# Optimization experiments

Hardware: AMD Instinct MI355X
Metric: run time of the kernel (lower is better)

The kernel has to match this reference:

```python
import jax, jax.numpy as jnp
import numpy as np

D_MODEL = 1024
D_HIDDEN = 4096
D_VOCAB = 32000
N_CTX = 2048
N_LAYERS = 8


def setup_inputs() -> dict:
    key = jax.random.key(0)
    ks = jax.random.split(key, 10)
    # scale params by 1/sqrt(fan_in) so softmax/logits are numerically sane
    s = 1.0 / np.sqrt(D_MODEL)
    sh = 1.0 / np.sqrt(D_HIDDEN)
    return {
        "tokens": jax.random.randint(ks[0], (N_CTX,), 0, D_VOCAB),
        "tok_emb": jax.random.normal(ks[1], (D_VOCAB, D_MODEL), jnp.float32) * s,
        "pos_emb": jax.random.normal(ks[2], (N_CTX, D_MODEL), jnp.float32) * s,
        "wqk": jax.random.normal(ks[3], (N_LAYERS, D_MODEL, D_MODEL), jnp.float32) * s,
        "wov": jax.random.normal(ks[4], (N_LAYERS, D_MODEL, D_MODEL), jnp.float32) * s,
        "w_up": jax.random.normal(ks[5], (N_LAYERS, D_HIDDEN, D_MODEL), jnp.float32) * s,
        "b_up": jax.random.normal(ks[6], (N_LAYERS, D_HIDDEN), jnp.float32) * 0.01,
        "w_down": jax.random.normal(ks[7], (N_LAYERS, D_MODEL, D_HIDDEN), jnp.float32) * sh,
        "b_down": jax.random.normal(ks[8], (N_LAYERS, D_MODEL), jnp.float32) * 0.01,
    }


def reference(tokens, tok_emb, pos_emb, wqk, wov, w_up, b_up, w_down, b_down):
    n = tokens.shape[0]
    # token + positional embedding  -> [n, d_model]
    x = tok_emb[tokens] + pos_emb[:n]
    # causal additive mask: -inf strictly above the diagonal
    idx = jnp.arange(n)
    mask = jnp.where(idx[None, :] > idx[:, None], -jnp.inf, 0.0).astype(x.dtype)
    for l in range(wqk.shape[0]):
        # MLP branch: relu(x W_up^T + b_up) W_down^T + b_down
        h = jnp.maximum(x @ w_up[l].T + b_up[l], 0.0) @ w_down[l].T + b_down[l]
        # attention branch: softmax(x Wqk x^T + M) x Wov
        scores = (x @ wqk[l]) @ x.T + mask          # [n, n]
        attn = jax.nn.softmax(scores, axis=-1) @ x @ wov[l]
        x = x + h + attn                             # parallel residual
    # tied unembedding -> logits [n, d_vocab]
    return x @ tok_emb.T
```

## Files before the change

kernel.cpp:

```cpp
#include <hip/hip_runtime.h>
#include <hip/hip_bf16.h>
#include <stdint.h>

#define DM 1024
#define DH 4096
#define DV 32000
#define NC 2048
#define NL 8

typedef float f32x4_t __attribute__((ext_vector_type(4)));
typedef __bf16 bf16x8_t __attribute__((ext_vector_type(8)));
typedef unsigned short u16x4_t __attribute__((ext_vector_type(4)));
typedef unsigned short u16x8_t __attribute__((ext_vector_type(8)));

typedef __attribute__((address_space(1))) void as1_void;
typedef __attribute__((address_space(3))) void as3_void;

__device__ __forceinline__ unsigned short f2bf(float f) {
  unsigned int u = __builtin_bit_cast(unsigned int, f);
  u += 0x7fffu + ((u >> 16) & 1u);
  return (unsigned short)(u >> 16);
}

__device__ __forceinline__ void gload_lds16(const void* g, void* l) {
  __builtin_amdgcn_global_load_lds((as1_void*)(void*)g, (as3_void*)l, 16, 0, 0);
}

template <int BNT, bool B_FP32, bool SPLIT, bool CAUSAL, bool CAUSAL_K,
          bool HAS_BIAS, bool RELU, bool OUT_BF16>
__device__ __forceinline__ void gemm_body(
    unsigned short* As, unsigned short* Bs, const unsigned short* __restrict__ A,
    const void* __restrict__ Bt, const float* __restrict__ bias,
    void* __restrict__ Cout, int M, int N, int lda, int Ks, int bx, int by,
    int koff, int zslice) {
  constexpr int BK = 64;
  constexpr int BN = BNT;
  constexpr int CPTA = 4;
  constexpr int CPTB = (BN * BK) / 2048;
  constexpr int NF = BN / 32;
  const int t = threadIdx.x;
  const int lane = t & 63;
  const int wid = t >> 6;
  const int wr = wid >> 1, wc = wid & 1;
  const int row0 = by * 128;
  const int col0 = bx * BN;

  if constexpr (CAUSAL) {
    if (col0 > row0 + 127) return;
  }

  int Kend = Ks;
  if constexpr (CAUSAL_K) {
    const int need = row0 + 128 - koff;
    Kend = need <= 0 ? 0 : (need >= Ks ? Ks : ((need + BK - 1) & ~(BK - 1)));
    if constexpr (SPLIT) {
      if (Kend <= 0) return;
    }
  }

  f32x4_t acc[4][NF];
#pragma unroll
  for (int m = 0; m < 4; m++)
#pragma unroll
    for (int n = 0; n < NF; n++) acc[m][n] = (f32x4_t){0.f, 0.f, 0.f, 0.f};

  for (int kt = 0; kt < Kend; kt += BK) {
    __syncthreads();
#pragma unroll
    for (int i = 0; i < CPTA; i++) {
      const int c = i * 256 + t;
      const int r = c >> 3;
      const int ko = ((c & 7) ^ (r & 7)) * 8;
      const unsigned short* g = A + (size_t)(row0 + r) * lda + koff + kt + ko;
      unsigned short* l = &As[(size_t)(i * 256 + wid * 64) * 8];
      gload_lds16(g, l);
    }
    if constexpr (B_FP32) {
      const float* Bf = (const float*)Bt;
#pragma unroll
      for (int i = 0; i < CPTB; i++) {
        const int c = i * 256 + t;
        const int r = c >> 3;
        const int ko = ((c & 7) ^ (r & 7)) * 8;
        const float* g = Bf + (size_t)(col0 + r) * lda + koff + kt + ko;
        const float4 f0 = *reinterpret_cast<const float4*>(g);
        const float4 f1 = *reinterpret_cast<const float4*>(g + 4);
        u16x8_t v;
        v[0] = f2bf(f0.x); v[1] = f2bf(f0.y); v[2] = f2bf(f0.z); v[3] = f2bf(f0.w);
        v[4] = f2bf(f1.x); v[5] = f2bf(f1.y); v[6] = f2bf(f1.z); v[7] = f2bf(f1.w);
        *reinterpret_cast<u16x8_t*>(&Bs[(size_t)c * 8]) = v;
      }
    } else {
      const unsigned short* Bu = (const unsigned short*)Bt;
#pragma unroll
      for (int i = 0; i < CPTB; i++) {
        const int c = i * 256 + t;
        const int r = c >> 3;
        const int ko = ((c & 7) ^ (r & 7)) * 8;
        const unsigned short* g = Bu + (size_t)(col0 + r) * lda + koff + kt + ko;
        unsigned short* l = &Bs[(size_t)(i * 256 + wid * 64) * 8];
        gload_lds16(g, l);
      }
    }
    __syncthreads();

#pragma unroll
    for (int kk = 0; kk < 2; kk++) {
      bf16x8_t av[4], bv[NF];
#pragma unroll
      for (int m = 0; m < 4; m++) {
        const int arow = wr * 64 + m * 16 + (lane & 15);
        const int akc = (kk * 4 + (lane >> 4)) ^ (arow & 7);
        av[m] = __builtin_bit_cast(
            bf16x8_t, *reinterpret_cast<const u16x8_t*>(&As[arow * BK + akc * 8]));
      }
#pragma unroll
      for (int n = 0; n < NF; n++) {
        const int brow = wc * (BN / 2) + n * 16 + (lane & 15);
        const int bkc = (kk * 4 + (lane >> 4)) ^ (brow & 7);
        bv[n] = __builtin_bit_cast(
            bf16x8_t, *reinterpret_cast<const u16x8_t*>(&Bs[brow * BK + bkc * 8]));
      }
#pragma unroll
      for (int m = 0; m < 4; m++)
#pragma unroll
        for (int n = 0; n < NF; n++)
          acc[m][n] = __builtin_amdgcn_mfma_f32_16x16x32_bf16(av[m], bv[n],
                                                              acc[m][n], 0, 0, 0);
    }
  }

#pragma unroll
  for (int m = 0; m < 4; m++) {
    const int rbase = row0 + wr * 64 + m * 16 + (lane >> 4) * 4;
#pragma unroll
    for (int n = 0; n < NF; n++) {
      const int col = col0 + wc * (BN / 2) + n * 16 + (lane & 15);
      if constexpr (SPLIT) {
        float* out = (float*)Cout + (size_t)zslice * M * N;
#pragma unroll
        for (int j = 0; j < 4; j++)
          out[(size_t)(rbase + j) * N + col] = acc[m][n][j];
      } else {
        float bval = 0.0f;
        if constexpr (HAS_BIAS) bval = bias[col];
#pragma unroll
        for (int j = 0; j < 4; j++) {
          float v = acc[m][n][j];
          if constexpr (HAS_BIAS) v += bval;
          if constexpr (RELU) v = fmaxf(v, 0.0f);
          const size_t idx = (size_t)(rbase + j) * N + col;
          if constexpr (OUT_BF16)
            ((unsigned short*)Cout)[idx] = f2bf(v);
          else
            __builtin_nontemporal_store(v, (float*)Cout + idx);
        }
      }
    }
  }
}

__device__ __forceinline__ void super_decode(int idx, int gy, int& bx, int& by) {
  const int s = idx >> 4;
  const int u = idx & 15;
  const int sgy = gy >> 2;
  const int sx = s / sgy;
  const int sy = s - sx * sgy;
  bx = sx * 4 + (u & 3);
  by = sy * 4 + (u >> 2);
}

template <int BNT, bool B_FP32, bool SPLIT, bool CAUSAL, bool CAUSAL_K,
          bool HAS_BIAS, bool RELU, bool OUT_BF16>
__global__ __launch_bounds__(256) void gemm_nt(
    const unsigned short* __restrict__ A, const void* __restrict__ Bt,
    const float* __restrict__ bias, void* __restrict__ Cout, int M, int N,
    int lda, int Ks) {
  __shared__ __attribute__((aligned(16))) unsigned short As[128 * 64];
  __shared__ __attribute__((aligned(16))) unsigned short Bs[BNT * 64];
  const int gx = gridDim.x, gy = gridDim.y;
  const int nwg = gx * gy;
  const int orig = blockIdx.y * gx + blockIdx.x;
  const int qq = nwg >> 3, rr = nwg & 7;
  const int xc = orig & 7, ii = orig >> 3;
  const int wgid = (xc < rr ? xc * (qq + 1) : rr * (qq + 1) + (xc - rr) * qq) + ii;
  int bx, by;
  super_decode(wgid, gy, bx, by);
  gemm_body<BNT, B_FP32, SPLIT, CAUSAL, CAUSAL_K, HAS_BIAS, RELU, OUT_BF16>(
      As, Bs, A, Bt, bias, Cout, M, N, lda, Ks, bx, by,
      SPLIT ? blockIdx.z * Ks : 0, blockIdx.z);
}

__global__ __launch_bounds__(256) void fused_up_q(
    const unsigned short* __restrict__ xb, const unsigned short* __restrict__ wupB,
    const float* __restrict__ bup, unsigned short* __restrict__ h1,
    const unsigned short* __restrict__ wqkT, float* __restrict__ qpool) {
  __shared__ __attribute__((aligned(16))) unsigned short As[128 * 64];
  __shared__ __attribute__((aligned(16))) unsigned short Bs[64 * 64];
  const int orig = blockIdx.x;
  const int xc = orig & 7, ii = orig >> 3;
  int bx, by;
  if (ii < 128) {
    const int idx = xc * 128 + ii;
    super_decode(idx, 16, bx, by);
    gemm_body<64, false, false, false, false, true, true, true>(
        As, Bs, xb, wupB, bup, h1, NC, DH, DM, DM, bx, by, 0, 0);
  } else {
    const int idx = xc * 64 + (ii - 128);
    const int z = idx >> 8;
    super_decode(idx & 255, 16, bx, by);
    gemm_body<64, false, true, false, false, false, false, false>(
        As, Bs, xb, wqkT, nullptr, qpool, NC, DM, DM, DM / 2, bx, by,
        z * (DM / 2), z);
  }
}

__global__ __launch_bounds__(256) void fused_down_rq(
    const unsigned short* __restrict__ h1, const unsigned short* __restrict__ wdownB,
    float* __restrict__ dpart, const float* __restrict__ qpool,
    unsigned short* __restrict__ qb) {
  __shared__ __attribute__((aligned(16))) unsigned short As[128 * 64];
  __shared__ __attribute__((aligned(16))) unsigned short Bs[64 * 64];
  const int orig = blockIdx.x;
  const int xc = orig & 7, ii = orig >> 3;
  if (ii < 128) {
    const int idx = xc * 128 + ii;
    const int z = idx >> 8;
    int bx, by;
    super_decode(idx & 255, 16, bx, by);
    gemm_body<64, false, true, false, false, false, false, false>(
        As, Bs, h1, wdownB, nullptr, dpart, NC, DM, DH, DH / 4, bx, by,
        z * (DH / 4), z);
  } else {
    const int ridx = xc * 256 + (ii - 128);
    const size_t nMD = (size_t)NC * DM;
    const size_t i = ((size_t)ridx * 256 + threadIdx.x) * 4;
    if (i < nMD) {
      float4 v = *reinterpret_cast<const float4*>(qpool + i);
      const float4 w = *reinterpret_cast<const float4*>(qpool + nMD + i);
      v.x += w.x; v.y += w.y; v.z += w.z; v.w += w.w;
      u16x4_t o;
      o[0] = f2bf(v.x); o[1] = f2bf(v.y); o[2] = f2bf(v.z); o[3] = f2bf(v.w);
      *reinterpret_cast<u16x4_t*>(qb + i) = o;
    }
  }
}

__global__ __launch_bounds__(256) void cast3_f32_bf16(
    const float* __restrict__ in0, unsigned short* __restrict__ out0, size_t n0,
    const float* __restrict__ in1, unsigned short* __restrict__ out1, size_t n1,
    const float* __restrict__ in2, unsigned short* __restrict__ out2, size_t n2,
    int gper) {
  const int seg = blockIdx.x / gper;
  const int lb = blockIdx.x - seg * gper;
  const float* in = seg == 0 ? in0 : (seg == 1 ? in1 : in2);
  unsigned short* out = seg == 0 ? out0 : (seg == 1 ? out1 : out2);
  const size_t n = seg == 0 ? n0 : (seg == 1 ? n1 : n2);
  const size_t stride = (size_t)gper * 256 * 8;
  for (size_t i = ((size_t)lb * 256 + threadIdx.x) * 8; i < n; i += stride) {
    const float4 a = *reinterpret_cast<const float4*>(in + i);
    const float4 b = *reinterpret_cast<const float4*>(in + i + 4);
    u16x8_t v;
    v[0] = f2bf(a.x); v[1] = f2bf(a.y); v[2] = f2bf(a.z); v[3] = f2bf(a.w);
    v[4] = f2bf(b.x); v[5] = f2bf(b.y); v[6] = f2bf(b.z); v[7] = f2bf(b.w);
    *reinterpret_cast<u16x8_t*>(out + i) = v;
  }
}

__global__ __launch_bounds__(256) void embed_kernel(
    const int* __restrict__ tokens, const float* __restrict__ tok_emb,
    const float* __restrict__ pos_emb, float* __restrict__ x,
    unsigned short* __restrict__ xb) {
  const int i = blockIdx.x;
  const int tok = tokens[i];
  const float* te = tok_emb + (size_t)tok * DM;
  const float* pe = pos_emb + (size_t)i * DM;
  float* xr = x + (size_t)i * DM;
  unsigned short* xbr = xb + (size_t)i * DM;
  const int j = threadIdx.x * 4;
  const float4 a = *reinterpret_cast<const float4*>(te + j);
  const float4 b = *reinterpret_cast<const float4*>(pe + j);
  float4 v;
  v.x = a.x + b.x; v.y = a.y + b.y; v.z = a.z + b.z; v.w = a.w + b.w;
  *reinterpret_cast<float4*>(xr + j) = v;
  u16x4_t o;
  o[0] = f2bf(v.x); o[1] = f2bf(v.y); o[2] = f2bf(v.z); o[3] = f2bf(v.w);
  *reinterpret_cast<u16x4_t*>(xbr + j) = o;
}

__global__ void transpose_cast_dual(const float* __restrict__ in0,
                                    unsigned short* __restrict__ out0,
                                    const float* __restrict__ in1,
                                    unsigned short* __restrict__ out1, int R,
                                    int C, int ZSPLIT) {
  __shared__ float tile[32][33];
  const int z = blockIdx.z;
  const float* in = (z < ZSPLIT) ? in0 : in1;
  unsigned short* out = (z < ZSPLIT) ? out0 : out1;
  const int zl = (z < ZSPLIT) ? z : z - ZSPLIT;
  const size_t lo = (size_t)zl * R * C;
  const int x = blockIdx.x * 32 + threadIdx.x;
#pragma unroll
  for (int i = threadIdx.y; i < 32; i += 8) {
    const int y = blockIdx.y * 32 + i;
    tile[i][threadIdx.x] = in[lo + (size_t)y * C + x];
  }
  __syncthreads();
  const int ox = blockIdx.y * 32 + threadIdx.x;
#pragma unroll
  for (int i = threadIdx.y; i < 32; i += 8) {
    const int oy = blockIdx.x * 32 + i;
    out[lo + (size_t)oy * R + ox] = f2bf(tile[threadIdx.x][i]);
  }
}

__global__ void transpose_u16(const unsigned short* __restrict__ in,
                              unsigned short* __restrict__ out, int R, int C) {
  __shared__ unsigned short tile[32][33];
  const int x = blockIdx.x * 32 + threadIdx.x;
#pragma unroll
  for (int i = threadIdx.y; i < 32; i += 8) {
    const int y = blockIdx.y * 32 + i;
    tile[i][threadIdx.x] = in[(size_t)y * C + x];
  }
  __syncthreads();
  const int ox = blockIdx.y * 32 + threadIdx.x;
#pragma unroll
  for (int i = threadIdx.y; i < 32; i += 8) {
    const int oy = blockIdx.x * 32 + i;
    out[(size_t)oy * R + ox] = tile[threadIdx.x][i];
  }
}

__global__ __launch_bounds__(256) void softmax_split2(
    const float* __restrict__ p0, const float* __restrict__ p1,
    unsigned short* __restrict__ P, int n) {
  __shared__ float srow[NC];
  __shared__ float sred[4];
  const int i = blockIdx.x;
  const int valid = i + 1;
  const int wlimit = (i & ~127) + 128;
  const int t = threadIdx.x;
  const int wid = t >> 6, lane = t & 63;
  const size_t ro = (size_t)i * n;
  for (int j = t; j < valid; j += 256) srow[j] = p0[ro + j] + p1[ro + j];
  __syncthreads();

  float m = -3.0e38f;
  for (int j = t; j < valid; j += 256) m = fmaxf(m, srow[j]);
#pragma unroll
  for (int o = 32; o > 0; o >>= 1) m = fmaxf(m, __shfl_xor(m, o, 64));
  if (lane == 0) sred[wid] = m;
  __syncthreads();
  m = fmaxf(fmaxf(sred[0], sred[1]), fmaxf(sred[2], sred[3]));
  __syncthreads();

  float s = 0.f;
  for (int j = t; j < valid; j += 256) s += __expf(srow[j] - m);
#pragma unroll
  for (int o = 32; o > 0; o >>= 1) s += __shfl_xor(s, o, 64);
  if (lane == 0) sred[wid] = s;
  __syncthreads();
  s = sred[0] + sred[1] + sred[2] + sred[3];
  const float inv = 1.0f / s;

  unsigned short* prow = P + ro;
  for (int j = t; j < wlimit; j += 256)
    prow[j] = (j < valid) ? f2bf(__expf(srow[j] - m) * inv) : (unsigned short)0;
}

__global__ __launch_bounds__(256) void softmax_causal(
    const float* __restrict__ S, unsigned short* __restrict__ P, int n) {
  __shared__ float srow[NC];
  __shared__ float sred[4];
  const int i = blockIdx.x;
  const int valid = i + 1;
  const int t = threadIdx.x;
  const int wid = t >> 6, lane = t & 63;
  const size_t ro = (size_t)i * n;
  for (int j = t; j < valid; j += 256) srow[j] = S[ro + j];
  __syncthreads();
  float m = -3.0e38f;
  for (int j = t; j < valid; j += 256) m = fmaxf(m, srow[j]);
#pragma unroll
  for (int o = 32; o > 0; o >>= 1) m = fmaxf(m, __shfl_xor(m, o, 64));
  if (lane == 0) sred[wid] = m;
  __syncthreads();
  m = fmaxf(fmaxf(sred[0], sred[1]), fmaxf(sred[2], sred[3]));
  __syncthreads();
  float s = 0.f;
  for (int j = t; j < valid; j += 256) s += __expf(srow[j] - m);
#pragma unroll
  for (int o = 32; o > 0; o >>= 1) s += __shfl_xor(s, o, 64);
  if (lane == 0) sred[wid] = s;
  __syncthreads();
  s = sred[0] + sred[1] + sred[2] + sred[3];
  const float inv = 1.0f / s;
  unsigned short* prow = P + ro;
  for (int j = t; j < n; j += 256)
    prow[j] = (j < valid) ? f2bf(__expf(srow[j] - m) * inv) : (unsigned short)0;
}

template <int NS>
__global__ __launch_bounds__(256) void reduce_to_bf16(
    const float* __restrict__ part, unsigned short* __restrict__ out, size_t n,
    size_t stride) {
  const size_t i = ((size_t)blockIdx.x * 256 + threadIdx.x) * 4;
  if (i >= n) return;
  float4 v = *reinterpret_cast<const float4*>(part + i);
#pragma unroll
  for (int s = 1; s < NS; s++) {
    const float4 w = *reinterpret_cast<const float4*>(part + (size_t)s * stride + i);
    v.x += w.x; v.y += w.y; v.z += w.z; v.w += w.w;
  }
  u16x4_t o;
  o[0] = f2bf(v.x); o[1] = f2bf(v.y); o[2] = f2bf(v.z); o[3] = f2bf(v.w);
  *reinterpret_cast<u16x4_t*>(out + i) = o;
}

__global__ __launch_bounds__(256) void reduce_pv_causal(
    const float* __restrict__ part, unsigned short* __restrict__ out, size_t n,
    size_t stride) {
  const size_t i = ((size_t)blockIdx.x * 256 + threadIdx.x) * 4;
  if (i >= n) return;
  const int row = (int)(i >> 10);
  const int nsl = (row >> 9) + 1;
  float4 v = *reinterpret_cast<const float4*>(part + i);
  for (int s = 1; s < nsl; s++) {
    const float4 w = *reinterpret_cast<const float4*>(part + (size_t)s * stride + i);
    v.x += w.x; v.y += w.y; v.z += w.z; v.w += w.w;
  }
  u16x4_t o;
  o[0] = f2bf(v.x); o[1] = f2bf(v.y); o[2] = f2bf(v.z); o[3] = f2bf(v.w);
  *reinterpret_cast<u16x4_t*>(out + i) = o;
}

__global__ __launch_bounds__(256) void residual_tiled(
    float* __restrict__ x, unsigned short* __restrict__ xb,
    unsigned short* __restrict__ xT, const float* __restrict__ dp,
    const float* __restrict__ op, const float* __restrict__ bd) {
  __shared__ unsigned short tile[32][33];
  const int tx = threadIdx.x;
  const int ty = threadIdx.y;
  const int col0 = blockIdx.x * 32;
  const int row0 = blockIdx.y * 32;
  const size_t n = (size_t)NC * DM;
  const int row = row0 + ty;
  const int col = col0 + tx * 4;
  const size_t idx = (size_t)row * DM + col;

  float4 v = *reinterpret_cast<const float4*>(x + idx);
  const float4 b = *reinterpret_cast<const float4*>(bd + col);
  v.x += b.x; v.y += b.y; v.z += b.z; v.w += b.w;
#pragma unroll
  for (int s = 0; s < 4; s++) {
    const float4 w = *reinterpret_cast<const float4*>(dp + (size_t)s * n + idx);
    v.x += w.x; v.y += w.y; v.z += w.z; v.w += w.w;
  }
#pragma unroll
  for (int s = 0; s < 2; s++) {
    const float4 w = *reinterpret_cast<const float4*>(op + (size_t)s * n + idx);
    v.x += w.x; v.y += w.y; v.z += w.z; v.w += w.w;
  }
  *reinterpret_cast<float4*>(x + idx) = v;
  u16x4_t o;
  o[0] = f2bf(v.x); o[1] = f2bf(v.y); o[2] = f2bf(v.z); o[3] = f2bf(v.w);
  *reinterpret_cast<u16x4_t*>(xb + idx) = o;
  tile[ty][tx * 4 + 0] = o[0];
  tile[ty][tx * 4 + 1] = o[1];
  tile[ty][tx * 4 + 2] = o[2];
  tile[ty][tx * 4 + 3] = o[3];
  __syncthreads();

  const int t = ty * 8 + tx;
  const int wc = t >> 5;
  const int wr = t & 31;
#pragma unroll
  for (int j = 0; j < 4; j++) {
    const int c = wc + j * 8;
    xT[(size_t)(col0 + c) * NC + row0 + wr] = tile[wr][c];
  }
}

__global__ __launch_bounds__(256) void residual_kernel(
    float* __restrict__ x, const float* __restrict__ hd,
    const float* __restrict__ attn, unsigned short* __restrict__ xb, int n) {
  const int idx = blockIdx.x * 256 + threadIdx.x;
  if (idx < n) {
    const float v = x[idx] + hd[idx] + attn[idx];
    x[idx] = v;
    xb[idx] = f2bf(v);
  }
}

extern "C" void kernel_launch(void* const* d_in, const int* in_sizes, int n_in,
                              void* d_out, int out_size, void* d_ws,
                              size_t ws_size, hipStream_t stream) {
  const int* tokens = (const int*)d_in[0];
  const float* tok_emb = (const float*)d_in[1];
  const float* pos_emb = (const float*)d_in[2];
  const float* wqk = (const float*)d_in[3];
  const float* wov = (const float*)d_in[4];
  const float* w_up = (const float*)d_in[5];
  const float* b_up = (const float*)d_in[6];
  const float* w_down = (const float*)d_in[7];
  const float* b_down = (const float*)d_in[8];
  float* logits = (float*)d_out;

  uint8_t* base = (uint8_t*)d_ws;
  size_t used = 0;
  auto alloc = [&](size_t bytes) -> void* {
    const size_t ab = (bytes + 255) & ~(size_t)255;
    if (used + ab > ws_size) return (void*)0;
    void* r = base + used;
    used += ab;
    return r;
  };

  float* x = (float*)alloc((size_t)NC * DM * 4);
  unsigned short* xb = (unsigned short*)alloc((size_t)NC * DM * 2);
  unsigned short* h1 = (unsigned short*)alloc((size_t)NC * DH * 2);
  unsigned short* qb = (unsigned short*)alloc((size_t)NC * DM * 2);
  unsigned short* Pb = (unsigned short*)alloc((size_t)NC * NC * 2);
  unsigned short* xT = (unsigned short*)alloc((size_t)NC * DM * 2);
  unsigned short* ab = (unsigned short*)alloc((size_t)NC * DM * 2);
  unsigned short* wqkT = (unsigned short*)alloc((size_t)NL * DM * DM * 2);
  unsigned short* wovT = (unsigned short*)alloc((size_t)NL * DM * DM * 2);
  float* hd = (float*)alloc((size_t)NC * DM * 4);
  float* attn = (float*)alloc((size_t)NC * DM * 4);
  float* scores = (float*)alloc((size_t)NC * NC * 4);
  float* dpart = (float*)alloc((size_t)4 * NC * DM * 4);
  float* opart = (float*)alloc((size_t)2 * NC * DM * 4);
  float* pool = (float*)alloc((size_t)2 * NC * NC * 4);
  unsigned short* wupB = (unsigned short*)alloc((size_t)NL * DH * DM * 2);
  unsigned short* wdownB = (unsigned short*)alloc((size_t)NL * DM * DH * 2);
  unsigned short* tokB = (unsigned short*)alloc((size_t)DV * DM * 2);

  const bool split_en = (dpart && opart && pool);
  const bool have_wbf = (wupB && wdownB);
  const bool have_tok = (tokB != 0);
  const bool fused_en = split_en && have_wbf;

  const dim3 tb(32, 8);
  transpose_cast_dual<<<dim3(DM / 32, DM / 32, 2 * NL), tb, 0, stream>>>(
      wqk, wqkT, wov, wovT, DM, DM, NL);
  if (have_wbf && have_tok) {
    cast3_f32_bf16<<<3 * 2048, 256, 0, stream>>>(
        w_up, wupB, (size_t)NL * DH * DM, w_down, wdownB, (size_t)NL * DM * DH,
        tok_emb, tokB, (size_t)DV * DM, 2048);
  }
  embed_kernel<<<NC, 256, 0, stream>>>(tokens, tok_emb, pos_emb, x, xb);
  transpose_u16<<<dim3(DM / 32, NC / 32), tb, 0, stream>>>(xb, xT, NC, DM);

  const size_t nMD = (size_t)NC * DM;

  for (int l = 0; l < NL; l++) {
    if (fused_en) {
      fused_up_q<<<1536, 256, 0, stream>>>(
          xb, wupB + (size_t)l * DH * DM, b_up + (size_t)l * DH, h1,
          wqkT + (size_t)l * DM * DM, pool);
      fused_down_rq<<<3072, 256, 0, stream>>>(
          h1, wdownB + (size_t)l * DM * DH, dpart, pool, qb);
    } else {
      gemm_nt<64, true, false, false, false, true, true, true>
          <<<dim3(DH / 64, NC / 128), 256, 0, stream>>>(
              xb, w_up + (size_t)l * DH * DM, b_up + (size_t)l * DH, h1, NC, DH, DM, DM);
      gemm_nt<64, true, false, false, false, true, false, false>
          <<<dim3(DM / 64, NC / 128), 256, 0, stream>>>(
              h1, w_down + (size_t)l * DM * DH, b_down + (size_t)l * DM, hd, NC, DM, DH, DH);
      gemm_nt<64, false, false, false, false, false, false, true>
          <<<dim3(DM / 64, NC / 128), 256, 0, stream>>>(
              xb, wqkT + (size_t)l * DM * DM, nullptr, qb, NC, DM, DM, DM);
    }

    if (split_en) {
      gemm_nt<64, false, true, true, false, false, false, false>
          <<<dim3(NC / 64, NC / 128, 2), 256, 0, stream>>>(
              qb, xb, nullptr, pool, NC, NC, DM, DM / 2);
      softmax_split2<<<NC, 256, 0, stream>>>(pool, pool + (size_t)NC * NC, Pb, NC);
    } else {
      gemm_nt<64, false, false, true, false, false, false, false>
          <<<dim3(NC / 64, NC / 128), 256, 0, stream>>>(
              qb, xb, nullptr, scores, NC, NC, DM, DM);
      softmax_causal<<<NC, 256, 0, stream>>>(scores, Pb, NC);
    }

    if (!split_en)
      transpose_u16<<<dim3(DM / 32, NC / 32), tb, 0, stream>>>(xb, xT, NC, DM);

    if (split_en) {
      gemm_nt<64, false, true, false, true, false, false, false>
          <<<dim3(DM / 64, NC / 128, 4), 256, 0, stream>>>(
              Pb, xT, nullptr, pool, NC, DM, NC, NC / 4);
      reduce_pv_causal<<<(nMD / 4 + 255) / 256, 256, 0, stream>>>(pool, ab, nMD, nMD);
    } else {
      gemm_nt<64, false, false, false, true, false, false, true>
          <<<dim3(DM / 64, NC / 128), 256, 0, stream>>>(
              Pb, xT, nullptr, ab, NC, DM, NC, NC);
    }

    if (split_en) {
      gemm_nt<64, false, true, false, false, false, false, false>
          <<<dim3(DM / 64, NC / 128, 2), 256, 0, stream>>>(
              ab, wovT + (size_t)l * DM * DM, nullptr, opart, NC, DM, DM, DM / 2);
      residual_tiled<<<dim3(DM / 32, NC / 32), dim3(8, 32), 0, stream>>>(
          x, xb, xT, dpart, opart, b_down + (size_t)l * DM);
    } else {
      gemm_nt<64, false, false, false, false, false, false, false>
          <<<dim3(DM / 64, NC / 128), 256, 0, stream>>>(
              ab, wovT + (size_t)l * DM * DM, nullptr, attn, NC, DM, DM, DM);
      residual_kernel<<<(int)(nMD / 256), 256, 0, stream>>>(x, hd, attn, xb, (int)nMD);
    }
  }

  if (have_tok)
    gemm_nt<64, false, false, false, false, false, false, false>
        <<<dim3(DV / 64, NC / 128), 256, 0, stream>>>(
            xb, tokB, nullptr, logits, NC, DV, DM, DM);
  else
    gemm_nt<64, true, false, false, false, false, false, false>
        <<<dim3(DV / 64, NC / 128), 256, 0, stream>>>(
            xb, tok_emb, nullptr, logits, NC, DV, DM, DM);
}
```

Baseline: 1.433 ms.

## Use 128x128-tile 512-thread GEMM kernel for final vocab unembedding

Adds a dedicated 512-thread GEMM kernel with 128x128 output tiles and uses it for the logits projection instead of the 256-thread 128x64 kernel. The larger N tile halves how often the activation A tile is reloaded per output column and raises MFMA work per LDS load. Output is written with nontemporal stores so the large logits tensor does not pollute cache. The grid is padded to 252 column blocks with early exit for out-of-range tiles, and the kernel is single-buffered with no prefetch, so latency hiding relies on occupancy.

```diff
diff --git a/kernel.cpp b/kernel.cpp
--- a/kernel.cpp
+++ b/kernel.cpp
@@ -189,6 +189,115 @@
   gemm_body<BNT, B_FP32, SPLIT, CAUSAL, CAUSAL_K, HAS_BIAS, RELU, OUT_BF16>(
       As, Bs, A, Bt, bias, Cout, M, N, lda, Ks, bx, by,
       SPLIT ? blockIdx.z * Ks : 0, blockIdx.z);
+}
+
+template <bool B_FP32>
+__global__ __launch_bounds__(512) void gemm_nt512(
+    const unsigned short* __restrict__ A, const void* __restrict__ Bt,
+    float* __restrict__ Cout, int M, int N, int lda, int Ks) {
+  __shared__ __attribute__((aligned(16))) unsigned short As[128 * 64];
+  __shared__ __attribute__((aligned(16))) unsigned short Bs[128 * 64];
+  const int gx = gridDim.x, gy = gridDim.y;
+  const int nwg = gx * gy;
+  const int orig = blockIdx.y * gx + blockIdx.x;
+  const int qq = nwg >> 3, rr = nwg & 7;
+  const int xc = orig & 7, ii = orig >> 3;
+  const int wgid = (xc < rr ? xc * (qq + 1) : rr * (qq + 1) + (xc - rr) * qq) + ii;
+  int bx, by;
+  super_decode(wgid, gy, bx, by);
+  if (bx * 128 >= N) return;
+
+  const int t = threadIdx.x;
+  const int lane = t & 63;
+  const int wid = t >> 6;
+  const int wr = wid >> 2, wc = wid & 3;
+  const int row0 = by * 128;
+  const int col0 = bx * 128;
+
+  f32x4_t acc[4][2];
+#pragma unroll
+  for (int m = 0; m < 4; m++)
+#pragma unroll
+    for (int n = 0; n < 2; n++) acc[m][n] = (f32x4_t){0.f, 0.f, 0.f, 0.f};
+
+  for (int kt = 0; kt < Ks; kt += 64) {
+    __syncthreads();
+#pragma unroll
+    for (int i = 0; i < 2; i++) {
+      const int c = i * 512 + t;
+      const int r = c >> 3;
+      const int ko = ((c & 7) ^ (r & 7)) * 8;
+      const unsigned short* g = A + (size_t)(row0 + r) * lda + kt + ko;
+      unsigned short* l = &As[(size_t)(i * 512 + wid * 64) * 8];
+      gload_lds16(g, l);
+    }
+    if constexpr (B_FP32) {
+      const float* Bf = (const float*)Bt;
+#pragma unroll
+      for (int i = 0; i < 2; i++) {
+        const int c = i * 512 + t;
+        const int r = c >> 3;
+        const int ko = ((c & 7) ^ (r & 7)) * 8;
+        const float* g = Bf + (size_t)(col0 + r) * lda + kt + ko;
+        const float4 f0 = *reinterpret_cast<const float4*>(g);
+        const float4 f1 = *reinterpret_cast<const float4*>(g + 4);
+        u16x8_t v;
+        v[0] = f2bf(f0.x); v[1] = f2bf(f0.y); v[2] = f2bf(f0.z); v[3] = f2bf(f0.w);
+        v[4] = f2bf(f1.x); v[5] = f2bf(f1.y); v[6] = f2bf(f1.z); v[7] = f2bf(f1.w);
+        *reinterpret_cast<u16x8_t*>(&Bs[(size_t)c * 8]) = v;
+      }
+    } else {
+      const unsigned short* Bu = (const unsigned short*)Bt;
+#pragma unroll
+      for (int i = 0; i < 2; i++) {
+        const int c = i * 512 + t;
+        const int r = c >> 3;
+        const int ko = ((c & 7) ^ (r & 7)) * 8;
+        const unsigned short* g = Bu + (size_t)(col0 + r) * lda + kt + ko;
+        unsigned short* l = &Bs[(size_t)(i * 512 + wid * 64) * 8];
+        gload_lds16(g, l);
+      }
+    }
+    __syncthreads();
+
+#pragma unroll
+    for (int kk = 0; kk < 2; kk++) {
+      bf16x8_t av[4], bv[2];
+#pragma unroll
+      for (int m = 0; m < 4; m++) {
+        const int arow = wr * 64 + m * 16 + (lane & 15);
+        const int akc = (kk * 4 + (lane >> 4)) ^ (arow & 7);
+        av[m] = __builtin_bit_cast(
+            bf16x8_t, *reinterpret_cast<const u16x8_t*>(&As[arow * 64 + akc * 8]));
+      }
+#pragma unroll
+      for (int n = 0; n < 2; n++) {
+        const int brow = wc * 32 + n * 16 + (lane & 15);
+        const int bkc = (kk * 4 + (lane >> 4)) ^ (brow & 7);
+        bv[n] = __builtin_bit_cast(
+            bf16x8_t, *reinterpret_cast<const u16x8_t*>(&Bs[brow * 64 + bkc * 8]));
+      }
+#pragma unroll
+      for (int m = 0; m < 4; m++)
+#pragma unroll
+        for (int n = 0; n < 2; n++)
+          acc[m][n] = __builtin_amdgcn_mfma_f32_16x16x32_bf16(av[m], bv[n],
+                                                              acc[m][n], 0, 0, 0);
+    }
+  }
+
+#pragma unroll
+  for (int m = 0; m < 4; m++) {
+    const int rbase = row0 + wr * 64 + m * 16 + (lane >> 4) * 4;
+#pragma unroll
+    for (int n = 0; n < 2; n++) {
+      const int col = col0 + wc * 32 + n * 16 + (lane & 15);
+#pragma unroll
+      for (int j = 0; j < 4; j++)
+        __builtin_nontemporal_store(acc[m][n][j],
+                                    Cout + (size_t)(rbase + j) * N + col);
+    }
+  }
 }
 
 __global__ __launch_bounds__(256) void fused_up_q(
@@ -614,11 +723,9 @@
   }
 
   if (have_tok)
-    gemm_nt<64, false, false, false, false, false, false, false>
-        <<<dim3(DV / 64, NC / 128), 256, 0, stream>>>(
-            xb, tokB, nullptr, logits, NC, DV, DM, DM);
+    gemm_nt512<false><<<dim3(252, NC / 128), 512, 0, stream>>>(
+        xb, tokB, logits, NC, DV, DM, DM);
   else
-    gemm_nt<64, true, false, false, false, false, false, false>
-        <<<dim3(DV / 64, NC / 128), 256, 0, stream>>>(
-            xb, tok_emb, nullptr, logits, NC, DV, DM, DM);
-}
+    gemm_nt512<true><<<dim3(252, NC / 128), 512, 0, stream>>>(
+        xb, tok_emb, logits, NC, DV, DM, DM);
+}
```

Measured after the change: 1.443 ms. About the same (+0.7%).

## Overlap per-layer weight and embedding bf16 casts with fused GEMM kernels

Applied to the files above, without the earlier changes.

The upfront cast now converts only layer 0's up/down weights. The next layer's weights and slices of the token embedding are converted by extra workgroups appended to the fused up/Q and down/reduce kernels. The goal is to hide the large fp32-to-bf16 conversion traffic behind GEMM compute instead of paying for it serially before the layers. In exchange, the extra memory-bound blocks compete with the GEMMs for bandwidth and CUs, and correctness depends on every layer's weights being cast in the kernel before they are used.

```diff
diff --git a/kernel.cpp b/kernel.cpp
--- a/kernel.cpp
+++ b/kernel.cpp
@@ -24,6 +24,20 @@
 
 __device__ __forceinline__ void gload_lds16(const void* g, void* l) {
   __builtin_amdgcn_global_load_lds((as1_void*)(void*)g, (as3_void*)l, 16, 0, 0);
+}
+
+__device__ __forceinline__ void cast_tail8(const float* __restrict__ src,
+                                           unsigned short* __restrict__ dst,
+                                           size_t n, int cidx, int tid) {
+  for (size_t i = (size_t)cidx * 2048 + (size_t)tid * 8; i < n;
+       i += (size_t)512 * 2048) {
+    const float4 a = *reinterpret_cast<const float4*>(src + i);
+    const float4 b = *reinterpret_cast<const float4*>(src + i + 4);
+    u16x8_t v;
+    v[0] = f2bf(a.x); v[1] = f2bf(a.y); v[2] = f2bf(a.z); v[3] = f2bf(a.w);
+    v[4] = f2bf(b.x); v[5] = f2bf(b.y); v[6] = f2bf(b.z); v[7] = f2bf(b.w);
+    *reinterpret_cast<u16x8_t*>(dst + i) = v;
+  }
 }
 
 template <int BNT, bool B_FP32, bool SPLIT, bool CAUSAL, bool CAUSAL_K,
@@ -194,7 +208,9 @@
 __global__ __launch_bounds__(256) void fused_up_q(
     const unsigned short* __restrict__ xb, const unsigned short* __restrict__ wupB,
     const float* __restrict__ bup, unsigned short* __restrict__ h1,
-    const unsigned short* __restrict__ wqkT, float* __restrict__ qpool) {
+    const unsigned short* __restrict__ wqkT, float* __restrict__ qpool,
+    const float* __restrict__ c0s, unsigned short* __restrict__ c0d, size_t c0n,
+    const float* __restrict__ c1s, unsigned short* __restrict__ c1d, size_t c1n) {
   __shared__ __attribute__((aligned(16))) unsigned short As[128 * 64];
   __shared__ __attribute__((aligned(16))) unsigned short Bs[64 * 64];
   const int orig = blockIdx.x;
@@ -205,20 +221,26 @@
     super_decode(idx, 16, bx, by);
     gemm_body<64, false, false, false, false, true, true, true>(
         As, Bs, xb, wupB, bup, h1, NC, DH, DM, DM, bx, by, 0, 0);
-  } else {
+  } else if (ii < 192) {
     const int idx = xc * 64 + (ii - 128);
     const int z = idx >> 8;
     super_decode(idx & 255, 16, bx, by);
     gemm_body<64, false, true, false, false, false, false, false>(
         As, Bs, xb, wqkT, nullptr, qpool, NC, DM, DM, DM / 2, bx, by,
         z * (DM / 2), z);
+  } else {
+    const int cidx = xc * 64 + (ii - 192);
+    cast_tail8(c0s, c0d, c0n, cidx, threadIdx.x);
+    cast_tail8(c1s, c1d, c1n, cidx, threadIdx.x);
   }
 }
 
 __global__ __launch_bounds__(256) void fused_down_rq(
     const unsigned short* __restrict__ h1, const unsigned short* __restrict__ wdownB,
     float* __restrict__ dpart, const float* __restrict__ qpool,
-    unsigned short* __restrict__ qb) {
+    unsigned short* __restrict__ qb,
+    const float* __restrict__ c0s, unsigned short* __restrict__ c0d, size_t c0n,
+    const float* __restrict__ c1s, unsigned short* __restrict__ c1d, size_t c1n) {
   __shared__ __attribute__((aligned(16))) unsigned short As[128 * 64];
   __shared__ __attribute__((aligned(16))) unsigned short Bs[64 * 64];
   const int orig = blockIdx.x;
@@ -231,7 +253,7 @@
     gemm_body<64, false, true, false, false, false, false, false>(
         As, Bs, h1, wdownB, nullptr, dpart, NC, DM, DH, DH / 4, bx, by,
         z * (DH / 4), z);
-  } else {
+  } else if (ii < 384) {
     const int ridx = xc * 256 + (ii - 128);
     const size_t nMD = (size_t)NC * DM;
     const size_t i = ((size_t)ridx * 256 + threadIdx.x) * 4;
@@ -243,6 +265,10 @@
       o[0] = f2bf(v.x); o[1] = f2bf(v.y); o[2] = f2bf(v.z); o[3] = f2bf(v.w);
       *reinterpret_cast<u16x4_t*>(qb + i) = o;
     }
+  } else {
+    const int cidx = xc * 64 + (ii - 384);
+    cast_tail8(c0s, c0d, c0n, cidx, threadIdx.x);
+    cast_tail8(c1s, c1d, c1n, cidx, threadIdx.x);
   }
 }
 
@@ -544,7 +570,11 @@
   const dim3 tb(32, 8);
   transpose_cast_dual<<<dim3(DM / 32, DM / 32, 2 * NL), tb, 0, stream>>>(
       wqk, wqkT, wov, wovT, DM, DM, NL);
-  if (have_wbf && have_tok) {
+  if (fused_en) {
+    cast3_f32_bf16<<<2 * 1024, 256, 0, stream>>>(
+        w_up, wupB, (size_t)DH * DM, w_down, wdownB, (size_t)DM * DH,
+        nullptr, nullptr, 0, 1024);
+  } else if (have_wbf && have_tok) {
     cast3_f32_bf16<<<3 * 2048, 256, 0, stream>>>(
         w_up, wupB, (size_t)NL * DH * DM, w_down, wdownB, (size_t)NL * DM * DH,
         tok_emb, tokB, (size_t)DV * DM, 2048);
@@ -553,14 +583,29 @@
   transpose_u16<<<dim3(DM / 32, NC / 32), tb, 0, stream>>>(xb, xT, NC, DM);
 
   const size_t nMD = (size_t)NC * DM;
+  const size_t tokQ = (size_t)DV * DM / (2 * NL);
 
   for (int l = 0; l < NL; l++) {
     if (fused_en) {
-      fused_up_q<<<1536, 256, 0, stream>>>(
+      const bool nw = (l + 1 < NL);
+      const float* u0s = nw ? w_up + (size_t)(l + 1) * DH * DM : nullptr;
+      unsigned short* u0d = nw ? wupB + (size_t)(l + 1) * DH * DM : nullptr;
+      const size_t u0n = nw ? (size_t)DH * DM : 0;
+      const float* d0s = nw ? w_down + (size_t)(l + 1) * DM * DH : nullptr;
+      unsigned short* d0d = nw ? wdownB + (size_t)(l + 1) * DM * DH : nullptr;
+      const size_t d0n = nw ? (size_t)DM * DH : 0;
+      const float* t0s = have_tok ? tok_emb + (size_t)l * 2 * tokQ : nullptr;
+      unsigned short* t0d = have_tok ? tokB + (size_t)l * 2 * tokQ : nullptr;
+      const float* t1s = have_tok ? tok_emb + (size_t)l * 2 * tokQ + tokQ : nullptr;
+      unsigned short* t1d = have_tok ? tokB + (size_t)l * 2 * tokQ + tokQ : nullptr;
+      const size_t tn = have_tok ? tokQ : 0;
+
+      fused_up_q<<<2048, 256, 0, stream>>>(
           xb, wupB + (size_t)l * DH * DM, b_up + (size_t)l * DH, h1,
-          wqkT + (size_t)l * DM * DM, pool);
-      fused_down_rq<<<3072, 256, 0, stream>>>(
-          h1, wdownB + (size_t)l * DM * DH, dpart, pool, qb);
+          wqkT + (size_t)l * DM * DM, pool, u0s, u0d, u0n, t0s, t0d, tn);
+      fused_down_rq<<<3584, 256, 0, stream>>>(
+          h1, wdownB + (size_t)l * DM * DH, dpart, pool, qb, d0s, d0d, d0n,
+          t1s, t1d, tn);
     } else {
       gemm_nt<64, true, false, false, false, true, true, true>
           <<<dim3(DH / 64, NC / 128), 256, 0, stream>>>(
@@ -613,7 +658,11 @@
     }
   }
 
-  if (have_tok)
+  if (fused_en && have_tok)
+    gemm_nt<64, false, false, false, false, false, false, false>
+        <<<dim3(DV / 64, NC / 128), 256, 0, stream>>>(
+            xb, tokB, nullptr, logits, NC, DV, DM, DM);
+  else if (have_tok)
     gemm_nt<64, false, false, false, false, false, false, false>
         <<<dim3(DV / 64, NC / 128), 256, 0, stream>>>(
             xb, tokB, nullptr, logits, NC, DV, DM, DM);
```

New measurement: 1.355 ms. 1.06x faster.
